# Kernel optimization log

Hardware: AMD Instinct MI355X
Metric: run time of the kernel (lower is better)

## Reference

```python
import jax, jax.numpy as jnp
import numpy as np

B, FIN, V, X, Y, Z = 2, 32, 768, 8, 8, 8
K, FOUT = 5, 32
NNZ = V * 8  # ~8 neighbors per vertex


def setup_inputs() -> dict:
    key = jax.random.key(0)
    k1, k2, k3, k4, k5 = jax.random.split(key, 5)
    std = np.sqrt(2.0 / (FIN * K)).astype(np.float32)
    return {
        "lap_rows": jax.random.randint(k1, (NNZ,), 0, V, dtype=jnp.int32),
        "lap_cols": jax.random.randint(k2, (NNZ,), 0, V, dtype=jnp.int32),
        "lap_vals": jax.random.normal(k3, (NNZ,), dtype=jnp.float32) * 0.1,
        "x": jax.random.normal(k4, (B, FIN, V, X, Y, Z), dtype=jnp.float32),
        "weight": jax.random.normal(k5, (K, FIN, FOUT), dtype=jnp.float32) * std,
        "bias": jnp.full((FOUT,), 0.01, dtype=jnp.float32),
    }


def reference(lap_rows, lap_cols, lap_vals, x, weight, bias):
    Bb, Fin, Vv, Xx, Yy, Zz = x.shape
    Kk, _, Fout = weight.shape

    def spmm(v):  # sparse [V,V] @ dense [V,D]
        return jax.ops.segment_sum(lap_vals[:, None] * v[lap_cols],
                                   lap_rows, num_segments=Vv)

    # [B,Fin,V,X,Y,Z] -> [V, Fin*B*X*Y*Z]
    x0 = jnp.transpose(x, (2, 1, 0, 3, 4, 5)).reshape(Vv, -1)
    xs = [x0]
    if Kk > 1:
        x1 = spmm(x0)
        xs.append(x1)
        for _ in range(2, Kk):
            x2 = 2.0 * spmm(x1) - x0
            xs.append(x2)
            x0, x1 = x1, x2
    basis = jnp.stack(xs, axis=0)  # [K, V, Fin*B*X*Y*Z]
    basis = basis.reshape(Kk, Vv, Fin, Bb, Xx, Yy, Zz)
    basis = jnp.transpose(basis, (3, 1, 4, 5, 6, 0, 2))  # [B,V,X,Y,Z,K,Fin]
    out = basis.reshape(-1, Kk * Fin) @ weight.reshape(Kk * Fin, Fout)
    out = out.reshape(Bb, Vv, Xx, Yy, Zz, Fout)
    out = jnp.transpose(out, (0, 5, 1, 2, 3, 4))  # [B,Fout,V,X,Y,Z]
    return out + bias[None, :, None, None, None, None]
```

## Files before the change

kernel.cpp:

```cpp
#include <hip/hip_runtime.h>
#include <stdint.h>

#define V      768
#define FINC   32
#define FOUTC  32
#define XYZ    512
#define NB     2
#define ROWP   40
#define MAXDEG 32
#define EROWS  36

typedef unsigned short u16;
typedef unsigned int   u32;
typedef short bf16x8 __attribute__((ext_vector_type(8)));
typedef float f32x4  __attribute__((ext_vector_type(4)));
typedef float f32x2  __attribute__((ext_vector_type(2)));

__device__ __forceinline__ u16 f2bf(float f) {
  u32 u = __float_as_uint(f);
  u32 r = u + 0x7fffu + ((u >> 16) & 1u);
  return (u16)(r >> 16);
}
__device__ __forceinline__ float bflo(u32 w) { return __uint_as_float(w << 16); }
__device__ __forceinline__ float bfhi(u32 w) { return __uint_as_float(w & 0xffff0000u); }
__device__ __forceinline__ float bfhi_raw(u32 w) { return __uint_as_float(w); }
__device__ __forceinline__ u32 cvtpk_bf16(float lo, float hi) {
  u32 r;
  asm("v_cvt_pk_bf16_f32 %0, %1, %2" : "=v"(r) : "v"(lo), "v"(hi));
  return r;
}

__global__ __launch_bounds__(64) void build_ell(const int* __restrict__ rows,
                                                const int* __restrict__ cols,
                                                const float* __restrict__ vals,
                                                int nnz,
                                                int2* __restrict__ epair,
                                                int* __restrict__ deg) {
  int v = blockIdx.x;
  int lane = threadIdx.x;
  int cnt = 0;
  for (int base = 0; base < nnz; base += 64) {
    int i = base + lane;
    bool m = (i < nnz) && (rows[i] == v);
    unsigned long long mask = __ballot(m);
    if (m) {
      int pos = cnt + __popcll(mask & ((1ull << lane) - 1ull));
      if (pos < MAXDEG)
        epair[v * MAXDEG + pos] = make_int2(cols[i], __float_as_int(vals[i]));
    }
    cnt += __popcll(mask);
  }
  int d = cnt < MAXDEG ? cnt : MAXDEG;
  for (int p = d + lane; p < MAXDEG; p += 64)
    epair[v * MAXDEG + p] = make_int2(0, 0);
  if (lane == 0) deg[v] = d;
}

__global__ __launch_bounds__(V) void sort_rows(const int2* __restrict__ epair,
                                               const int* __restrict__ deg,
                                               int2* __restrict__ ep3,
                                               int* __restrict__ perm,
                                               int* __restrict__ inv_g,
                                               int* __restrict__ wtrip) {
  __shared__ int sdeg[V];
  __shared__ u16 sinv[V];
  int v = threadIdx.x;
  int d = deg[v];
  sdeg[v] = d;
  __syncthreads();
  int r = 0;
  for (int u = 0; u < V; ++u) {
    int du = sdeg[u];
    r += (du > d) || (du == d && u < v);
  }
  const unsigned long long GPK = 0x8495A6B73210ull;
  int w = (int)((GPK >> (4 * (r >> 6))) & 15ull);
  int p = w * 64 + (r & 63);
  perm[p] = v;
  inv_g[v] = p;
  sinv[v] = (u16)p;
  if ((r & 63) == 0) wtrip[w] = d;
  __syncthreads();
  for (int e = 0; e < EROWS; ++e) {
    int2 o = make_int2(0, 0);
    if (e < d) {
      int2 pe = epair[v * MAXDEG + e];
      o = make_int2((int)sinv[pe.x] * (ROWP * 2), pe.y);
    }
    ep3[e * V + p] = o;
  }
}

#define TXV 12
__global__ __launch_bounds__(512) void transpose_x(const float* __restrict__ x,
                                                   const int* __restrict__ perm,
                                                   u16* __restrict__ xT) {
  __shared__ u16 TL[384][66];
  __shared__ int PV[TXV];
  int g = blockIdx.x;
  int b = g >> 9, pvt = (g >> 3) & 63, xt = g & 7;
  int pv0 = pvt * TXV;
  int xyz0 = xt * 64;
  int t = threadIdx.x;
  if (t < TXV) PV[t] = perm[pv0 + t];
  __syncthreads();
  int lane = t & 63, pg = t >> 6;
#pragma unroll
  for (int st = 0; st < 48; ++st) {
    int pair = st * 8 + pg;
    int vloc = pair >> 5, f = pair & 31;
    float val = x[((size_t)(b * FINC + f) * V + PV[vloc]) * XYZ + xyz0 + lane];
    TL[pair][lane] = f2bf(val);
  }
  __syncthreads();
  int s = t & 7, xyz = t >> 3;
  u32* dst = (u32*)(xT + ((size_t)(b * XYZ + xyz0 + xyz) * V + pv0) * FINC);
#pragma unroll
  for (int it = 0; it < 24; ++it) {
    int i = s + 8 * it;
    u32 lo = TL[2 * i][xyz], hi = TL[2 * i + 1][xyz];
    dst[i] = lo | (hi << 16);
  }
}

__global__ __launch_bounds__(1024, 4) void cheb_main(
    const u16* __restrict__ xT, const int2* __restrict__ ep3,
    const int* __restrict__ perm, const int* __restrict__ wtrip,
    const float* __restrict__ weight, const float* __restrict__ bias,
    u32* __restrict__ stage) {
  __shared__ __align__(16) u16   CUR[V * ROWP];
  __shared__ __align__(16) u16   PRV[V * ROWP];
  __shared__ __align__(16) uint4 WF[5][2][64];
  __shared__ u16 PRM[V];
  __shared__ int WT[12];

  int g = blockIdx.x;
  int xcd = g & 7;
  int u = g >> 3;
  int phase = u >> 5;
  int xyz = xcd * 32 + (u & 31) + (phase & 1) * 256;
  int b = phase >> 1;
  int slice = b * XYZ + xyz;

  int tid = threadIdx.x;
  int lane = tid & 63;
  int w = tid >> 6;
  int l15 = lane & 15, l4 = lane >> 4;
  bool gath = tid < V;

  if (tid < 640) {
    int k = tid >> 7, n = (tid >> 6) & 1, ln = tid & 63;
    int a15 = ln & 15, a4 = ln >> 4;
    u32 pw[4];
#pragma unroll
    for (int p = 0; p < 4; ++p) {
      float w0 = weight[(size_t)(k * FINC + a4 * 8 + 2 * p) * FOUTC + n * 16 + a15];
      float w1 = weight[(size_t)(k * FINC + a4 * 8 + 2 * p + 1) * FOUTC + n * 16 + a15];
      pw[p] = (u32)f2bf(w0) | ((u32)f2bf(w1) << 16);
    }
    WF[k][n][ln] = make_uint4(pw[0], pw[1], pw[2], pw[3]);
  }
  if (tid < 12) WT[tid] = wtrip[tid];
  if (gath) PRM[tid] = (u16)perm[tid];
  float bsv[2] = {bias[l15], bias[16 + l15]};

  if (gath) {
    const uint4* src = (const uint4*)(xT + (size_t)slice * V * FINC) + tid * 4;
    uint4* dst = (uint4*)(CUR + tid * ROWP);
#pragma unroll
    for (int j = 0; j < 4; ++j) dst[j] = src[j];
  }
  __syncthreads();

  int trip = 0;
  if (w < 12) trip = __builtin_amdgcn_readfirstlane(WT[w]);
  const int2* pp = ep3 + tid;

  f32x4 acc[3][2];
#pragma unroll
  for (int a = 0; a < 3; ++a)
#pragma unroll
    for (int n = 0; n < 2; ++n) acc[a][n] = (f32x4){0.f, 0.f, 0.f, 0.f};

  auto gemm_acc = [&](int k) {
    bf16x8 bn0 = *(const bf16x8*)&WF[k][0][lane];
    bf16x8 bn1 = *(const bf16x8*)&WF[k][1][lane];
#pragma unroll
    for (int a = 0; a < 3; ++a) {
      int row = w * 48 + a * 16 + l15;
      bf16x8 af = *(const bf16x8*)(CUR + row * ROWP + l4 * 8);
      acc[a][0] = __builtin_amdgcn_mfma_f32_16x16x32_bf16(af, bn0, acc[a][0], 0, 0, 0);
      acc[a][1] = __builtin_amdgcn_mfma_f32_16x16x32_bf16(af, bn1, acc[a][1], 0, 0, 0);
    }
  };

  f32x2 fa2[16];
  auto fma_edge = [&](float fv, uint4 qa, uint4 qb, uint4 qc, uint4 qd) {
    f32x2 fv2 = {fv, fv};
    u32 wq[16] = {qa.x, qa.y, qa.z, qa.w, qb.x, qb.y, qb.z, qb.w,
                  qc.x, qc.y, qc.z, qc.w, qd.x, qd.y, qd.z, qd.w};
#pragma unroll
    for (int p = 0; p < 16; ++p) {
      f32x2 s = {bflo(wq[p]), bfhi_raw(wq[p])};
      fa2[p] += fv2 * s;
    }
  };
  auto gather = [&]() {
#pragma unroll
    for (int j = 0; j < 16; ++j) fa2[j] = (f32x2){0.f, 0.f};
    int trips = (trip + 1) & ~1;
    int2 r0 = pp[0], r1 = pp[V], r2 = pp[2 * V];
    const uint4* s0 = (const uint4*)((const char*)CUR + (u32)r0.x);
    uint4 A0 = s0[0], A1 = s0[1], A2 = s0[2], A3 = s0[3];
    for (int e = 0; e < trips; e += 2) {
      const uint4* s1 = (const uint4*)((const char*)CUR + (u32)r1.x);
      uint4 B0 = s1[0], B1 = s1[1], B2 = s1[2], B3 = s1[3];
      int2 n3 = pp[(e + 3) * V];
      fma_edge(__int_as_float(r0.y), A0, A1, A2, A3);
      const uint4* s2 = (const uint4*)((const char*)CUR + (u32)r2.x);
      A0 = s2[0]; A1 = s2[1]; A2 = s2[2]; A3 = s2[3];
      int2 n4 = pp[(e + 4) * V];
      fma_edge(__int_as_float(r1.y), B0, B1, B2, B3);
      r0 = r2; r1 = n3; r2 = n4;
    }
  };

  auto do_update = [&](bool first) {
    uint4* cp = (uint4*)(CUR + tid * ROWP);
    uint4* qp = (uint4*)(PRV + tid * ROWP);
    uint4 c[4];
#pragma unroll
    for (int j = 0; j < 4; ++j) c[j] = cp[j];
    u32 npk[16];
    if (first) {
#pragma unroll
      for (int j = 0; j < 16; ++j) npk[j] = cvtpk_bf16(fa2[j][0], fa2[j][1]);
    } else {
      uint4 pv[4];
#pragma unroll
      for (int j = 0; j < 4; ++j) pv[j] = qp[j];
      u32 wp[16] = {pv[0].x, pv[0].y, pv[0].z, pv[0].w, pv[1].x, pv[1].y, pv[1].z, pv[1].w,
                    pv[2].x, pv[2].y, pv[2].z, pv[2].w, pv[3].x, pv[3].y, pv[3].z, pv[3].w};
#pragma unroll
      for (int j = 0; j < 16; ++j) {
        float t0 = 2.f * fa2[j][0] - bflo(wp[j]);
        float t1 = 2.f * fa2[j][1] - bfhi(wp[j]);
        npk[j] = cvtpk_bf16(t0, t1);
      }
    }
#pragma unroll
    for (int j = 0; j < 4; ++j) {
      qp[j] = c[j];
      cp[j] = make_uint4(npk[4 * j], npk[4 * j + 1], npk[4 * j + 2], npk[4 * j + 3]);
    }
  };

#pragma unroll
  for (int ph = 0; ph <= 3; ++ph) {
    gemm_acc(ph);
    if (gath) gather();
    __syncthreads();
    if (gath) do_update(ph == 0);
    __syncthreads();
  }

  gemm_acc(4);

  u32* stg = stage + (size_t)slice * (V * 16);
#pragma unroll
  for (int a = 0; a < 3; ++a) {
#pragma unroll
    for (int r = 0; r < 4; ++r) {
      int vr = PRM[w * 48 + a * 16 + l4 * 4 + r];
      u32 pk = cvtpk_bf16(acc[a][0][r] + bsv[0], acc[a][1][r] + bsv[1]);
      stg[vr * 16 + l15] = pk;
    }
  }
}

#define TO_VT  12
#define TO_PAD 193
__global__ __launch_bounds__(512) void transpose_out(const u32* __restrict__ stage,
                                                     float* __restrict__ out) {
  __shared__ u32 T[64 * TO_PAD];
  int g = blockIdx.x;
  int b = g >> 9, vt = (g >> 3) & 63, xt = g & 7;
  int v0 = vt * TO_VT;
  int xyz0 = xt * 64;
  int t = threadIdx.x;
  const u32* base = stage + (size_t)(b * XYZ + xyz0) * (V * 16) + v0 * 16;
#pragma unroll
  for (int i = 0; i < 6; ++i) {
    int idx4 = i * 512 + t;
    int j = idx4 / 48;
    int c4 = idx4 - j * 48;
    uint4 q = *(const uint4*)(base + (size_t)j * (V * 16) + c4 * 4);
    int w0 = c4 * 4;
    T[j * TO_PAD + w0]     = q.x;
    T[j * TO_PAD + w0 + 1] = q.y;
    T[j * TO_PAD + w0 + 2] = q.z;
    T[j * TO_PAD + w0 + 3] = q.w;
  }
  __syncthreads();
  int wv = t >> 6, lane = t & 63;
#pragma unroll
  for (int i = 0; i < 48; ++i) {
    int fout = wv * 4 + i / 12;
    int vv = i % 12;
    u32 pk = T[lane * TO_PAD + vv * 16 + (fout & 15)];
    float val = (fout < 16) ? bflo(pk) : bfhi(pk);
    out[((size_t)(b * FOUTC + fout) * V + v0 + vv) * XYZ + xyz0 + lane] = val;
  }
}

extern "C" void kernel_launch(void* const* d_in, const int* in_sizes, int n_in,
                              void* d_out, int out_size, void* d_ws, size_t ws_size,
                              hipStream_t stream) {
  const int*   lap_rows = (const int*)d_in[0];
  const int*   lap_cols = (const int*)d_in[1];
  const float* lap_vals = (const float*)d_in[2];
  const float* x        = (const float*)d_in[3];
  const float* weight   = (const float*)d_in[4];
  const float* bias     = (const float*)d_in[5];
  float* out = (float*)d_out;
  int nnz = in_sizes[0];

  char* ws = (char*)d_ws;
  const size_t XT_BYTES = (size_t)NB * XYZ * V * FINC * sizeof(u16);
  const size_t EP_BYTES = (size_t)V * MAXDEG * 8;
  const size_t E3_BYTES = (size_t)EROWS * V * 8;
  u16*  xT    = (u16*)ws;
  u32*  stg   = (u32*)ws;
  int2* epair = (int2*)(ws + XT_BYTES);
  int2* ep3   = (int2*)(ws + XT_BYTES + EP_BYTES);
  int*  deg   = (int*)(ws + XT_BYTES + EP_BYTES + E3_BYTES);
  int*  perm  = (int*)(ws + XT_BYTES + EP_BYTES + E3_BYTES + 3072);
  int*  inv_g = (int*)(ws + XT_BYTES + EP_BYTES + E3_BYTES + 6144);
  int*  wtrip = (int*)(ws + XT_BYTES + EP_BYTES + E3_BYTES + 9216);

  hipLaunchKernelGGL(build_ell, dim3(V), dim3(64), 0, stream,
                     lap_rows, lap_cols, lap_vals, nnz, epair, deg);
  hipLaunchKernelGGL(sort_rows, dim3(1), dim3(V), 0, stream,
                     epair, deg, ep3, perm, inv_g, wtrip);
  hipLaunchKernelGGL(transpose_x, dim3(NB * 64 * 8), dim3(512), 0, stream,
                     x, perm, xT);
  hipLaunchKernelGGL(cheb_main, dim3(NB * XYZ), dim3(1024), 0, stream,
                     xT, ep3, perm, wtrip, weight, bias, stg);
  hipLaunchKernelGGL(transpose_out, dim3(NB * 64 * 8), dim3(512), 0, stream,
                     stg, out);
}
```

Before: 204.6 us.

## Move ELL permutation into transpose_x and vectorize transpose loads and stores

The serial per-row ELL remap loop moves out of the single-block sort_rows kernel. It is spread across the first 36 blocks of transpose_x, which read inv_g from global memory. transpose_x now loads x as float4 and packs to bf16 pairs with cvtpk_bf16, and transpose_out writes float2 pairs instead of scalar floats. This reduces serial work in the single-block kernel and the number of global memory transactions, at the cost of extra work in a few transpose blocks. The shared layout changes also alter the bank access patterns.

```diff
diff --git a/kernel.cpp b/kernel.cpp
--- a/kernel.cpp
+++ b/kernel.cpp
@@ -56,14 +56,11 @@
   if (lane == 0) deg[v] = d;
 }
 
-__global__ __launch_bounds__(V) void sort_rows(const int2* __restrict__ epair,
-                                               const int* __restrict__ deg,
-                                               int2* __restrict__ ep3,
+__global__ __launch_bounds__(V) void sort_rows(const int* __restrict__ deg,
                                                int* __restrict__ perm,
                                                int* __restrict__ inv_g,
                                                int* __restrict__ wtrip) {
   __shared__ int sdeg[V];
-  __shared__ u16 sinv[V];
   int v = threadIdx.x;
   int d = deg[v];
   sdeg[v] = d;
@@ -78,47 +75,59 @@
   int p = w * 64 + (r & 63);
   perm[p] = v;
   inv_g[v] = p;
-  sinv[v] = (u16)p;
   if ((r & 63) == 0) wtrip[w] = d;
-  __syncthreads();
-  for (int e = 0; e < EROWS; ++e) {
-    int2 o = make_int2(0, 0);
-    if (e < d) {
-      int2 pe = epair[v * MAXDEG + e];
-      o = make_int2((int)sinv[pe.x] * (ROWP * 2), pe.y);
-    }
-    ep3[e * V + p] = o;
-  }
 }
 
 #define TXV 12
 __global__ __launch_bounds__(512) void transpose_x(const float* __restrict__ x,
                                                    const int* __restrict__ perm,
+                                                   const int* __restrict__ deg,
+                                                   const int2* __restrict__ epair,
+                                                   const int* __restrict__ inv_g,
+                                                   int2* __restrict__ ep3,
                                                    u16* __restrict__ xT) {
-  __shared__ u16 TL[384][66];
+  __shared__ u32 TL2[384 * 34];
   __shared__ int PV[TXV];
   int g = blockIdx.x;
+  int t = threadIdx.x;
+  if (g < EROWS) {
+    int e = g;
+    for (int p = t; p < V; p += 512) {
+      int v = perm[p];
+      int d = deg[v];
+      int2 o = make_int2(0, 0);
+      if (e < d) {
+        int2 pe = epair[v * MAXDEG + e];
+        o = make_int2(inv_g[pe.x] * (ROWP * 2), pe.y);
+      }
+      ep3[e * V + p] = o;
+    }
+  }
   int b = g >> 9, pvt = (g >> 3) & 63, xt = g & 7;
   int pv0 = pvt * TXV;
   int xyz0 = xt * 64;
-  int t = threadIdx.x;
   if (t < TXV) PV[t] = perm[pv0 + t];
   __syncthreads();
-  int lane = t & 63, pg = t >> 6;
-#pragma unroll
-  for (int st = 0; st < 48; ++st) {
-    int pair = st * 8 + pg;
-    int vloc = pair >> 5, f = pair & 31;
-    float val = x[((size_t)(b * FINC + f) * V + PV[vloc]) * XYZ + xyz0 + lane];
-    TL[pair][lane] = f2bf(val);
-  }
-  __syncthreads();
+  int q = t & 15;
+  int rgrp = t >> 4;
+#pragma unroll
+  for (int st = 0; st < 12; ++st) {
+    int row = st * 32 + rgrp;
+    int vloc = row >> 5, f = row & 31;
+    const float4 xv = *(const float4*)&x[((size_t)(b * FINC + f) * V + PV[vloc]) * XYZ + xyz0 + 4 * q];
+    u32 A = cvtpk_bf16(xv.x, xv.y);
+    u32 B = cvtpk_bf16(xv.z, xv.w);
+    *(uint2*)&TL2[row * 34 + 2 * q] = make_uint2(A, B);
+  }
+  __syncthreads();
+  const u16* TL16 = (const u16*)TL2;
   int s = t & 7, xyz = t >> 3;
   u32* dst = (u32*)(xT + ((size_t)(b * XYZ + xyz0 + xyz) * V + pv0) * FINC);
 #pragma unroll
   for (int it = 0; it < 24; ++it) {
     int i = s + 8 * it;
-    u32 lo = TL[2 * i][xyz], hi = TL[2 * i + 1][xyz];
+    u32 lo = TL16[(2 * i) * 68 + xyz];
+    u32 hi = TL16[(2 * i + 1) * 68 + xyz];
     dst[i] = lo | (hi << 16);
   }
 }
@@ -302,14 +311,19 @@
     T[j * TO_PAD + w0 + 3] = q.w;
   }
   __syncthreads();
-  int wv = t >> 6, lane = t & 63;
-#pragma unroll
-  for (int i = 0; i < 48; ++i) {
-    int fout = wv * 4 + i / 12;
-    int vv = i % 12;
-    u32 pk = T[lane * TO_PAD + vv * 16 + (fout & 15)];
-    float val = (fout < 16) ? bflo(pk) : bfhi(pk);
-    out[((size_t)(b * FOUTC + fout) * V + v0 + vv) * XYZ + xyz0 + lane] = val;
+  int xyz2 = t & 31;
+  int grp = t >> 5;
+#pragma unroll
+  for (int i = 0; i < 24; ++i) {
+    int fout = grp * 2 + (i & 1);
+    int vv = i >> 1;
+    int col = vv * 16 + (fout & 15);
+    u32 pka = T[(2 * xyz2) * TO_PAD + col];
+    u32 pkb = T[(2 * xyz2 + 1) * TO_PAD + col];
+    float va = (fout < 16) ? bflo(pka) : bfhi(pka);
+    float vb = (fout < 16) ? bflo(pkb) : bfhi(pkb);
+    *(float2*)&out[((size_t)(b * FOUTC + fout) * V + v0 + vv) * XYZ + xyz0 + 2 * xyz2] =
+        make_float2(va, vb);
   }
 }
 
@@ -341,9 +355,9 @@
   hipLaunchKernelGGL(build_ell, dim3(V), dim3(64), 0, stream,
                      lap_rows, lap_cols, lap_vals, nnz, epair, deg);
   hipLaunchKernelGGL(sort_rows, dim3(1), dim3(V), 0, stream,
-                     epair, deg, ep3, perm, inv_g, wtrip);
+                     deg, perm, inv_g, wtrip);
   hipLaunchKernelGGL(transpose_x, dim3(NB * 64 * 8), dim3(512), 0, stream,
-                     x, perm, xT);
+                     x, perm, deg, epair, inv_g, ep3, xT);
   hipLaunchKernelGGL(cheb_main, dim3(NB * XYZ), dim3(1024), 0, stream,
                      xT, ep3, perm, wtrip, weight, bias, stg);
   hipLaunchKernelGGL(transpose_out, dim3(NB * 64 * 8), dim3(512), 0, stream,
```

Result: faster. 193.6 us (-5.4%).
